# Kernel optimization log

Hardware: AMD Instinct MI355X
Metric: run time of the kernel (lower is better)

The kernel has to match this reference:

```python
import jax, jax.numpy as jnp
import numpy as np
from math import factorial

# ---- static config mirroring Cace.__init__ ----
MAX_L = 3            # max angular degree
N_RBF = 8            # Bessel radial basis size
RB = 8               # n_radial_basis (radial embedding dim after transform)
K = 3                # n_atom_basis -> edge channels C = K*K
NZ = 4               # len(zs)
CUTOFF = 5.5
N_NODES = 2000
N_EDGES = 50000
T_MP = 1             # num_message_passing
MP_NORM = 1.0 / np.sqrt(25.0)   # 1/sqrt(avg_num_neighbors)
C = K * K

def _lxlylz(max_l):
    out = []
    for l in range(max_l + 1):
        for lx in range(l, -1, -1):
            for ly in range(l - lx, -1, -1):
                out.append((lx, ly, l - lx - ly))
    return out

L_LIST = _lxlylz(MAX_L)                 # 20 Cartesian monomials for max_l=3
NL = len(L_LIST)
LX = np.array([t[0] for t in L_LIST]); LY = np.array([t[1] for t in L_LIST]); LZ = np.array([t[2] for t in L_LIST])
DEGS = LX + LY + LZ                     # degree l of each monomial
MULTI = np.array([factorial(int(d)) / (factorial(int(a)) * factorial(int(b)) * factorial(int(c)))
                  for a, b, c, d in zip(LX, LY, LZ, DEGS)], dtype=np.float32)
SEL = np.zeros((NL, MAX_L + 1), np.float32)
SEL[np.arange(NL), DEGS] = 1.0          # monomial -> degree one-hot (for per-l sums)
NB = 1 + (MAX_L + 1)                    # symmetrizer feats: nu=1 (l=0) + nu=2 per l

def bessel(r):  # [E] -> [E, N_RBF]
    n = jnp.arange(1, N_RBF + 1, dtype=r.dtype)
    return jnp.sqrt(2.0 / CUTOFF) * jnp.sin(n[None, :] * jnp.pi * r[:, None] / CUTOFF) / r[:, None]

def poly_cutoff(r):  # MACE-style polynomial cutoff, p=6
    p = 6.0
    u = r / CUTOFF
    f = 1.0 - (p + 1.0) * (p + 2.0) / 2.0 * u**6 + p * (p + 2.0) * u**7 - p * (p + 1.0) / 2.0 * u**8
    return f * (u < 1.0)

def axis_pows(x):  # [E] -> [E, MAX_L+1] = x^0..x^MAX_L (safe grads, handles negatives)
    pows = [jnp.ones_like(x)]
    for _ in range(MAX_L):
        pows.append(pows[-1] * x)
    return jnp.stack(pows, axis=1)

def angular(u):  # unit vectors [E,3] -> Cartesian monomials [E, NL]
    return axis_pows(u[:, 0])[:, LX] * axis_pows(u[:, 1])[:, LY] * axis_pows(u[:, 2])[:, LZ]

def radial_transform(x, W):  # x [N,R,L,C], W [MAX_L+1,R,Rb] shared per degree l
    return jnp.einsum('nrlc,lrb->nblc', x, W[DEGS])

def symmetrize(A):  # A [N,Rb,NL,C] -> B [N,Rb,NB,C]
    b1 = A[:, :, :1, :]  # nu=1: the (0,0,0) monomial (index 0)
    w = (A * A) * jnp.asarray(MULTI)[None, None, :, None]
    b2 = jnp.einsum('nrlc,lm->nrmc', w, jnp.asarray(SEL))  # nu=2 invariant per degree l
    return jnp.concatenate([b1, b2], axis=2)


def setup_inputs() -> dict:
    key = jax.random.key(0)
    ks = jax.random.split(key, 9)
    positions = jax.random.uniform(ks[0], (N_NODES, 3), dtype=jnp.float32) * 12.0
    species = jax.random.randint(ks[1], (N_NODES,), 0, NZ)
    send = jax.random.randint(ks[2], (N_EDGES,), 0, N_NODES)
    off = jax.random.randint(ks[3], (N_EDGES,), 1, N_NODES)
    recv = (send + off) % N_NODES  # no self-edges -> strictly positive edge lengths
    edge_index = jnp.stack([send, recv])
    shifts = jnp.zeros((N_EDGES, 3), jnp.float32)
    W_embed = jax.random.normal(ks[4], (NZ, K), jnp.float32)
    W_radial = jax.random.normal(ks[5], (MAX_L + 1, N_RBF, RB), jnp.float32) / np.sqrt(N_RBF)
    W_mem = jax.random.normal(ks[6], (MAX_L + 1, RB, RB), jnp.float32) / np.sqrt(RB)
    W_ar = jax.random.normal(ks[7], (N_RBF, RB), jnp.float32) / np.sqrt(N_RBF)
    W_chi = jax.random.normal(ks[8], (RB, NB), jnp.float32) * 0.1
    return {"positions": positions, "shifts": shifts, "W_embed": W_embed, "W_radial": W_radial,
            "W_mem": W_mem, "W_ar": W_ar, "W_chi": W_chi, "species": species, "edge_index": edge_index}


def reference(positions, shifts, W_embed, W_radial, W_mem, W_ar, W_chi, species, edge_index):
    n_nodes = positions.shape[0]
    send, recv = edge_index[0], edge_index[1]
    # edge geometry
    vec = positions[recv] - positions[send] + shifts
    lengths = jnp.linalg.norm(vec, axis=-1)
    u = vec / (lengths[:, None] + 1e-9)
    rad = bessel(lengths)          # [E,R]
    fcut = poly_cutoff(lengths)    # [E]
    ang = angular(u)               # [E,NL]
    # edge type encoding: outer product of sender/receiver species embeddings
    emb = W_embed[species]         # [N,K]
    enc = (emb[send][:, :, None] * emb[recv][:, None, :]).reshape(-1, C)  # [E,C]
    # elementwise_multiply_3tensors -> [E,R,NL,C]
    edge_attri = jnp.einsum('er,el,ec->erlc', rad * fcut[:, None], ang, enc)
    A = radial_transform(jax.ops.segment_sum(edge_attri, recv, num_segments=n_nodes), W_radial)  # [N,Rb,NL,C]
    B = symmetrize(A)              # [N,Rb,NB,C]
    feats = [B]
    for _ in range(T_MP):
        mem = jnp.einsum('nrlc,lrb->nblc', A, W_mem[DEGS])        # NodeMemory
        chi = jnp.einsum('nbkc,bk->nc', B, W_chi)                  # MessageBchi node scalar
        msg_bchi = edge_attri * chi[send][:, None, None, :]
        A_bchi = radial_transform(jax.ops.segment_sum(msg_bchi, recv, num_segments=n_nodes), W_radial)
        fr = (rad @ W_ar) * fcut[:, None]                          # MessageAr radial filter [E,Rb]
        msg_ar = A[send] * fr[:, :, None, None]
        A_ar = jax.ops.segment_sum(msg_ar, recv, num_segments=n_nodes)
        A = (A_ar + A_bchi) * MP_NORM + mem
        B = symmetrize(A)
        feats.append(B)
    return jnp.stack(feats, axis=-1)   # [N,Rb,NB,C,T_MP+1]
```

## Files before the change

kernel.cpp:

```cpp
#include <hip/hip_runtime.h>
#include <hip/hip_bf16.h>


#define CUTF 5.5f
#define MPNORM 0.2f

__constant__ int   d_DEGS[20]  = {0,1,1,1,2,2,2,2,2,2,3,3,3,3,3,3,3,3,3,3};
__constant__ float d_MULTI[20] = {1,1,1,1,1,2,2,1,2,1,1,3,3,3,6,3,1,3,3,1};

__global__ __launch_bounds__(1024) void k_prep(const int* __restrict__ eidx,
                                               int* __restrict__ offs,
                                               int* __restrict__ cursor,
                                               int N, int E) {
  __shared__ int cnt[2048];
  __shared__ int part[1024];
  int t = threadIdx.x;
  cnt[t] = 0; cnt[t + 1024] = 0;
  for (int i = t; i < N; i += 1024) cursor[i] = 0;
  __syncthreads();
  const int* recv = eidx + E;
  if ((E & 3) == 0) {
    #pragma unroll 2
    for (int i = t * 4; i + 3 < E; i += 4096) {
      int4 v = *reinterpret_cast<const int4*>(recv + i);
      atomicAdd(&cnt[v.x], 1); atomicAdd(&cnt[v.y], 1);
      atomicAdd(&cnt[v.z], 1); atomicAdd(&cnt[v.w], 1);
    }
  } else {
    #pragma unroll 4
    for (int i = t; i < E; i += 1024) atomicAdd(&cnt[recv[i]], 1);
  }
  __syncthreads();
  int a = cnt[2 * t], b = cnt[2 * t + 1];
  int s = a + b;
  part[t] = s;
  __syncthreads();
  for (int d = 1; d < 1024; d <<= 1) {
    int add = (t >= d) ? part[t - d] : 0;
    __syncthreads();
    part[t] += add;
    __syncthreads();
  }
  int excl = part[t] - s;
  if (2 * t     < N) offs[2 * t]     = excl;
  if (2 * t + 1 < N) offs[2 * t + 1] = excl + a;
  if (t == 1023) offs[N] = part[1023];
}

__global__ void k_edge(const float* __restrict__ pos,
                       const float* __restrict__ shifts,
                       const float* __restrict__ Wemb,
                       const float* __restrict__ War,
                       const int* __restrict__ species,
                       const int* __restrict__ eidx,
                       const int* __restrict__ offs,
                       int* __restrict__ cursor,
                       float* __restrict__ edata,
                       int* __restrict__ esend,
                       int E) {
  __shared__ float war_s[64];
  int t = threadIdx.x;
  if (t < 64) war_s[t] = War[t];
  __syncthreads();
  int e = blockIdx.x * blockDim.x + t;
  if (e >= E) return;
  int s  = eidx[e];
  int rI = eidx[E + e];
  float vx = pos[rI*3+0] - pos[s*3+0] + shifts[e*3+0];
  float vy = pos[rI*3+1] - pos[s*3+1] + shifts[e*3+1];
  float vz = pos[rI*3+2] - pos[s*3+2] + shifts[e*3+2];
  float len = sqrtf(vx*vx + vy*vy + vz*vz);
  float inv = 1.0f / (len + 1e-9f);
  float ux = vx*inv, uy = vy*inv, uz = vz*inv;
  float uu = len * (1.0f/CUTF);
  float u2 = uu*uu, u6 = u2*u2*u2;
  float fcut = (uu < 1.0f) ? (1.0f - 28.0f*u6 + 48.0f*u6*uu - 21.0f*u6*u2) : 0.0f;
  float x = 3.14159265358979f * uu;
  float sn = sinf(x), c2 = 2.0f*cosf(x), snm1 = 0.0f;
  float pref = sqrtf(2.0f/CUTF) / (len + 1e-20f);
  float rad[8];
  float v[48];
  #pragma unroll
  for (int k = 0; k < 8; k++) {
    rad[k] = pref * sn;
    v[k]   = rad[k] * fcut;
    float nxt = c2*sn - snm1; snm1 = sn; sn = nxt;
  }
  #pragma unroll
  for (int b = 0; b < 8; b++) {
    float a = 0.0f;
    #pragma unroll
    for (int k = 0; k < 8; k++) a += rad[k] * war_s[k*8+b];
    v[8+b] = a * fcut;
  }
  float px2 = ux*ux, py2 = uy*uy, pz2 = uz*uz;
  v[16] = 1.0f; v[17] = ux;     v[18] = uy;     v[19] = uz;
  v[20] = px2;  v[21] = ux*uy;  v[22] = ux*uz;  v[23] = py2;
  v[24] = uy*uz;v[25] = pz2;
  v[26] = px2*ux; v[27] = px2*uy; v[28] = px2*uz; v[29] = ux*py2;
  v[30] = ux*uy*uz; v[31] = ux*pz2; v[32] = py2*uy; v[33] = py2*uz;
  v[34] = uy*pz2; v[35] = pz2*uz;
  int zs = species[s], zr = species[rI];
  float es0 = Wemb[zs*3+0], es1 = Wemb[zs*3+1], es2 = Wemb[zs*3+2];
  float er0 = Wemb[zr*3+0], er1 = Wemb[zr*3+1], er2 = Wemb[zr*3+2];
  v[36] = es0*er0; v[37] = es0*er1; v[38] = es0*er2;
  v[39] = es1*er0; v[40] = es1*er1; v[41] = es1*er2;
  v[42] = es2*er0; v[43] = es2*er1; v[44] = es2*er2;
  v[45] = 0.0f; v[46] = 0.0f; v[47] = 0.0f;
  int slot = atomicAdd(&cursor[rI], 1);
  int dst = offs[rI] + slot;
  float4* eb4 = reinterpret_cast<float4*>(edata + (size_t)dst * 48);
  #pragma unroll
  for (int w = 0; w < 12; w++)
    eb4[w] = make_float4(v[4*w], v[4*w+1], v[4*w+2], v[4*w+3]);
  esend[dst] = s;
}

__global__ __launch_bounds__(192) void k_nodeA(
    const float* __restrict__ edata, const int* __restrict__ offs,
    const float* __restrict__ Wrad, const float* __restrict__ Wchi,
    float* __restrict__ A, uint4* __restrict__ Abf2,
    float* __restrict__ chi, float* __restrict__ B0, int N) {
  __shared__ float wr_s[288];
  __shared__ float wchi_s[40];
  __shared__ float Bsh[360];
  int t = threadIdx.x, n = blockIdx.x;
  for (int i = t; i < 256; i += 192) { int d = i >> 6, rm = i & 63; wr_s[d*72+rm] = Wrad[i]; }
  for (int i = t; i < 40;  i += 192) wchi_s[i] = Wchi[i];
  for (int i = t; i < 360; i += 192) Bsh[i] = 0.0f;
  int l = t / 9, c = t - l*9;
  bool act = t < 180;
  int ll = act ? l : 0, cc = act ? c : 0;
  float acc[8];
  #pragma unroll
  for (int r = 0; r < 8; r++) acc[r] = 0.0f;
  int start = offs[n], end = offs[n+1];
  #pragma unroll 4
  for (int j = start; j < end; j++) {
    const float* row = edata + (size_t)j * 48;
    float p = row[16+ll] * row[36+cc];
    #pragma unroll
    for (int r = 0; r < 8; r++) acc[r] += row[r] * p;
  }
  __syncthreads();
  int deg = act ? d_DEGS[ll] : 0;
  const float* wp = &wr_s[deg*72];
  float Ab[8];
  #pragma unroll
  for (int b = 0; b < 8; b++) {
    float a = 0.0f;
    #pragma unroll
    for (int r = 0; r < 8; r++) a += acc[r] * wp[r*8+b];
    Ab[b] = a;
  }
  if (act) {
    #pragma unroll
    for (int b = 0; b < 8; b++) A[(size_t)n*1440 + t*8 + b] = Ab[b];
    unsigned int pk[4];
    #pragma unroll
    for (int bp = 0; bp < 4; bp++) {
      __hip_bfloat16 blo = __float2bfloat16(Ab[2*bp]);
      __hip_bfloat16 bhi = __float2bfloat16(Ab[2*bp+1]);
      pk[bp] = (unsigned int)(*reinterpret_cast<unsigned short*>(&blo))
             | ((unsigned int)(*reinterpret_cast<unsigned short*>(&bhi)) << 16);
    }
    uint4 q; q.x = pk[0]; q.y = pk[1]; q.z = pk[2]; q.w = pk[3];
    Abf2[(size_t)n*180 + t] = q;
    if (l == 0) {
      #pragma unroll
      for (int b = 0; b < 8; b++) Bsh[b*45 + c] = Ab[b];
    }
    float mlt = d_MULTI[ll]; int kk = 1 + deg;
    #pragma unroll
    for (int b = 0; b < 8; b++) atomicAdd(&Bsh[b*45 + kk*9 + c], mlt*Ab[b]*Ab[b]);
  }
  __syncthreads();
  if (t < 9) {
    float s = 0.0f;
    for (int b = 0; b < 8; b++)
      #pragma unroll
      for (int kq = 0; kq < 5; kq++) s += Bsh[b*45 + kq*9 + t] * wchi_s[b*5 + kq];
    chi[n*9 + t] = s;
  }
  for (int i = t; i < 360; i += 192)
    B0[(size_t)n*360 + i] = Bsh[i];
}

__global__ __launch_bounds__(192) void k_node2(
    const float* __restrict__ edata, const int* __restrict__ esend,
    const int* __restrict__ offs,
    const float* __restrict__ Wrad, const float* __restrict__ Wmem,
    const float* __restrict__ A, const uint4* __restrict__ Abf2,
    const float* __restrict__ chi, const float* __restrict__ B0,
    float* __restrict__ out, int N) {
  __shared__ float wr_s[288], wm_s[288];
  __shared__ float Bsh[360];
  int t = threadIdx.x, n = blockIdx.x;
  for (int i = t; i < 256; i += 192) {
    int d = i >> 6, rm = i & 63;
    wr_s[d*72+rm] = Wrad[i];
    wm_s[d*72+rm] = Wmem[i];
  }
  for (int i = t; i < 360; i += 192) Bsh[i] = 0.0f;
  int l = t / 9, c = t - l*9;
  bool act = t < 180;
  int ll = act ? l : 0, cc = act ? c : 0;
  int tt = act ? t : 0;
  float Sacc[8], ARacc[8];
  #pragma unroll
  for (int r = 0; r < 8; r++) { Sacc[r] = 0.0f; ARacc[r] = 0.0f; }
  int start = offs[n], end = offs[n+1];
  #pragma unroll 4
  for (int j = start; j < end; j++) {
    const float* row = edata + (size_t)j * 48;
    int snd = esend[j];
    float ch = chi[snd*9 + cc];
    float pch = row[16+ll] * row[36+cc] * ch;
    #pragma unroll
    for (int r = 0; r < 8; r++) Sacc[r] += row[r] * pch;
    const uint4 q = Abf2[(size_t)snd*180 + tt];
    float a0 = __uint_as_float(q.x << 16), a1 = __uint_as_float(q.x & 0xffff0000u);
    float a2 = __uint_as_float(q.y << 16), a3 = __uint_as_float(q.y & 0xffff0000u);
    float a4 = __uint_as_float(q.z << 16), a5 = __uint_as_float(q.z & 0xffff0000u);
    float a6 = __uint_as_float(q.w << 16), a7 = __uint_as_float(q.w & 0xffff0000u);
    ARacc[0] += a0*row[8];  ARacc[1] += a1*row[9];
    ARacc[2] += a2*row[10]; ARacc[3] += a3*row[11];
    ARacc[4] += a4*row[12]; ARacc[5] += a5*row[13];
    ARacc[6] += a6*row[14]; ARacc[7] += a7*row[15];
  }
  __syncthreads();
  if (act) {
    int deg = d_DEGS[ll];
    const float* wrp = &wr_s[deg*72];
    const float* wmp = &wm_s[deg*72];
    const float* aop = A + (size_t)n*1440 + t*8;
    float aown[8];
    #pragma unroll
    for (int r = 0; r < 8; r++) aown[r] = aop[r];
    float newA[8];
    #pragma unroll
    for (int b = 0; b < 8; b++) {
      float mem = 0.0f, ab = 0.0f;
      #pragma unroll
      for (int r = 0; r < 8; r++) { mem += aown[r]*wmp[r*8+b]; ab += Sacc[r]*wrp[r*8+b]; }
      newA[b] = (ARacc[b] + ab)*MPNORM + mem;
    }
    if (l == 0) {
      #pragma unroll
      for (int b = 0; b < 8; b++) Bsh[b*45 + c] = newA[b];
    }
    float mlt = d_MULTI[ll]; int kk = 1 + deg;
    #pragma unroll
    for (int b = 0; b < 8; b++) atomicAdd(&Bsh[b*45 + kk*9 + c], mlt*newA[b]*newA[b]);
  }
  __syncthreads();
  float2* out2 = reinterpret_cast<float2*>(out);
  for (int i = t; i < 360; i += 192) {
    float2 pk; pk.x = B0[(size_t)n*360 + i]; pk.y = Bsh[i];
    out2[(size_t)n*360 + i] = pk;
  }
}

extern "C" void kernel_launch(void* const* d_in, const int* in_sizes, int n_in,
                              void* d_out, int out_size, void* d_ws, size_t ws_size,
                              hipStream_t stream) {
  const float* pos    = (const float*)d_in[0];
  const float* shifts = (const float*)d_in[1];
  const float* Wemb   = (const float*)d_in[2];
  const float* Wrad   = (const float*)d_in[3];
  const float* Wmem   = (const float*)d_in[4];
  const float* War    = (const float*)d_in[5];
  const float* Wchi   = (const float*)d_in[6];
  const int* species = (const int*)d_in[7];
  const int* eidx    = (const int*)d_in[8];
  float* out = (float*)d_out;
  int N = in_sizes[7];
  int E = in_sizes[8] / 2;

  char* base = (char*)d_ws;
  size_t off = 0;
  float* edata = (float*)(base + off); off += (size_t)E*48*4;
  float* A     = (float*)(base + off); off += (size_t)N*1440*4;
  uint4* Abf2  = (uint4*)(base + off); off += (size_t)N*180*16;
  float* chi   = (float*)(base + off); off += (size_t)N*9*4;
  float* B0    = (float*)(base + off); off += (size_t)N*360*4;
  int* cursor  = (int*)(base + off);   off += (size_t)N*4;
  int* offs    = (int*)(base + off);   off += (((size_t)(N+1)*4) + 15) & ~(size_t)15;
  int* esend   = (int*)(base + off);   off += (size_t)E*4;

  int eb = (E + 255) / 256;
  k_prep<<<1, 1024, 0, stream>>>(eidx, offs, cursor, N, E);
  k_edge<<<eb, 256, 0, stream>>>(pos, shifts, Wemb, War, species, eidx, offs, cursor,
                                 edata, esend, E);
  k_nodeA<<<N, 192, 0, stream>>>(edata, offs, Wrad, Wchi, A, Abf2, chi, B0, N);
  k_node2<<<N, 192, 0, stream>>>(edata, esend, offs, Wrad, Wmem, A, Abf2, chi, B0, out, N);
}
```

Baseline: 151.8 us.

## Fuse node passes into one cooperative kernel with grid sync and register-held A

Replaces the two node kernels with a single cooperative kernel. Each block handles two nodes, keeps their A values in registers across a grid-wide sync, and writes both B outputs as packed float2 at the end. This removes one launch, the fp32 A round trip and the B0 round trip through global memory. In exchange it depends on every block being co-resident (1000 blocks of 192 threads), adds grid-barrier cost, and keeps the two-kernel path as a fallback.

```diff
diff --git a/kernel.cpp b/kernel.cpp
--- a/kernel.cpp
+++ b/kernel.cpp
@@ -1,9 +1,12 @@
 #include <hip/hip_runtime.h>
 #include <hip/hip_bf16.h>
+#include <hip/hip_cooperative_groups.h>
 
 
 #define CUTF 5.5f
 #define MPNORM 0.2f
+
+namespace cg = cooperative_groups;
 
 __constant__ int   d_DEGS[20]  = {0,1,1,1,2,2,2,2,2,2,3,3,3,3,3,3,3,3,3,3};
 __constant__ float d_MULTI[20] = {1,1,1,1,1,2,2,1,2,1,1,3,3,3,6,3,1,3,3,1};
@@ -116,6 +119,149 @@
   esend[dst] = s;
 }
 
+__global__ __launch_bounds__(192, 3) void k_nodeF(
+    const float* __restrict__ edata, const int* __restrict__ esend,
+    const int* __restrict__ offs,
+    const float* __restrict__ Wrad, const float* __restrict__ Wmem,
+    const float* __restrict__ Wchi,
+    uint4* __restrict__ Abf2, float* __restrict__ chi,
+    float* __restrict__ out, int N, int G) {
+  __shared__ float wr_s[288], wm_s[288];
+  __shared__ float wchi_s[40];
+  __shared__ float Bsh1[2][360];
+  __shared__ float Bsh2[360];
+  int t = threadIdx.x;
+  for (int i = t; i < 256; i += 192) {
+    int d = i >> 6, rm = i & 63;
+    wr_s[d*72+rm] = Wrad[i];
+    wm_s[d*72+rm] = Wmem[i];
+  }
+  for (int i = t; i < 40;  i += 192) wchi_s[i] = Wchi[i];
+  for (int i = t; i < 720; i += 192) (&Bsh1[0][0])[i] = 0.0f;
+  int l = t / 9, c = t - l*9;
+  bool act = t < 180;
+  int ll = act ? l : 0, cc = act ? c : 0;
+  int tt = act ? t : 0;
+  int deg = d_DEGS[ll];
+  float mlt = d_MULTI[ll];
+  int kk1 = 1 + deg;
+  __syncthreads();
+
+  float AbK[2][8];
+  #pragma unroll
+  for (int q = 0; q < 2; q++) {
+    int n = blockIdx.x + q * G;
+    if (n < N) {
+      float acc[8];
+      #pragma unroll
+      for (int r = 0; r < 8; r++) acc[r] = 0.0f;
+      int start = offs[n], end = offs[n+1];
+      #pragma unroll 4
+      for (int j = start; j < end; j++) {
+        const float* row = edata + (size_t)j * 48;
+        float p = row[16+ll] * row[36+cc];
+        #pragma unroll
+        for (int r = 0; r < 8; r++) acc[r] += row[r] * p;
+      }
+      const float* wp = &wr_s[deg*72];
+      #pragma unroll
+      for (int b = 0; b < 8; b++) {
+        float a = 0.0f;
+        #pragma unroll
+        for (int r = 0; r < 8; r++) a += acc[r] * wp[r*8+b];
+        AbK[q][b] = a;
+      }
+      if (act) {
+        unsigned int pk[4];
+        #pragma unroll
+        for (int bp = 0; bp < 4; bp++) {
+          __hip_bfloat16 blo = __float2bfloat16(AbK[q][2*bp]);
+          __hip_bfloat16 bhi = __float2bfloat16(AbK[q][2*bp+1]);
+          pk[bp] = (unsigned int)(*reinterpret_cast<unsigned short*>(&blo))
+                 | ((unsigned int)(*reinterpret_cast<unsigned short*>(&bhi)) << 16);
+        }
+        uint4 qq; qq.x = pk[0]; qq.y = pk[1]; qq.z = pk[2]; qq.w = pk[3];
+        Abf2[(size_t)n*180 + t] = qq;
+        if (l == 0) {
+          #pragma unroll
+          for (int b = 0; b < 8; b++) Bsh1[q][b*45 + c] = AbK[q][b];
+        }
+        #pragma unroll
+        for (int b = 0; b < 8; b++)
+          atomicAdd(&Bsh1[q][b*45 + kk1*9 + c], mlt*AbK[q][b]*AbK[q][b]);
+      }
+    }
+    __syncthreads();
+    if (n < N && t < 9) {
+      float s = 0.0f;
+      for (int b = 0; b < 8; b++)
+        #pragma unroll
+        for (int kq = 0; kq < 5; kq++) s += Bsh1[q][b*45 + kq*9 + t] * wchi_s[b*5 + kq];
+      chi[n*9 + t] = s;
+    }
+  }
+  __threadfence();
+  cg::this_grid().sync();
+  #pragma unroll
+  for (int q = 0; q < 2; q++) {
+    int n = blockIdx.x + q * G;
+    for (int i = t; i < 360; i += 192) Bsh2[i] = 0.0f;
+    __syncthreads();
+    if (n < N) {
+      float Sacc[8], ARacc[8];
+      #pragma unroll
+      for (int r = 0; r < 8; r++) { Sacc[r] = 0.0f; ARacc[r] = 0.0f; }
+      int start = offs[n], end = offs[n+1];
+      #pragma unroll 4
+      for (int j = start; j < end; j++) {
+        const float* row = edata + (size_t)j * 48;
+        int snd = esend[j];
+        float ch = chi[snd*9 + cc];
+        float pch = row[16+ll] * row[36+cc] * ch;
+        #pragma unroll
+        for (int r = 0; r < 8; r++) Sacc[r] += row[r] * pch;
+        const uint4 qv = Abf2[(size_t)snd*180 + tt];
+        float a0 = __uint_as_float(qv.x << 16), a1 = __uint_as_float(qv.x & 0xffff0000u);
+        float a2 = __uint_as_float(qv.y << 16), a3 = __uint_as_float(qv.y & 0xffff0000u);
+        float a4 = __uint_as_float(qv.z << 16), a5 = __uint_as_float(qv.z & 0xffff0000u);
+        float a6 = __uint_as_float(qv.w << 16), a7 = __uint_as_float(qv.w & 0xffff0000u);
+        ARacc[0] += a0*row[8];  ARacc[1] += a1*row[9];
+        ARacc[2] += a2*row[10]; ARacc[3] += a3*row[11];
+        ARacc[4] += a4*row[12]; ARacc[5] += a5*row[13];
+        ARacc[6] += a6*row[14]; ARacc[7] += a7*row[15];
+      }
+      if (act) {
+        const float* wrp = &wr_s[deg*72];
+        const float* wmp = &wm_s[deg*72];
+        float newA[8];
+        #pragma unroll
+        for (int b = 0; b < 8; b++) {
+          float mem = 0.0f, ab = 0.0f;
+          #pragma unroll
+          for (int r = 0; r < 8; r++) { mem += AbK[q][r]*wmp[r*8+b]; ab += Sacc[r]*wrp[r*8+b]; }
+          newA[b] = (ARacc[b] + ab)*MPNORM + mem;
+        }
+        if (l == 0) {
+          #pragma unroll
+          for (int b = 0; b < 8; b++) Bsh2[b*45 + c] = newA[b];
+        }
+        #pragma unroll
+        for (int b = 0; b < 8; b++)
+          atomicAdd(&Bsh2[b*45 + kk1*9 + c], mlt*newA[b]*newA[b]);
+      }
+    }
+    __syncthreads();
+    if (n < N) {
+      float2* out2 = reinterpret_cast<float2*>(out);
+      for (int i = t; i < 360; i += 192) {
+        float2 pk2; pk2.x = Bsh1[q][i]; pk2.y = Bsh2[i];
+        out2[(size_t)n*360 + i] = pk2;
+      }
+    }
+    __syncthreads();
+  }
+}
+
 __global__ __launch_bounds__(192) void k_nodeA(
     const float* __restrict__ edata, const int* __restrict__ offs,
     const float* __restrict__ Wrad, const float* __restrict__ Wchi,
@@ -164,8 +310,8 @@
       pk[bp] = (unsigned int)(*reinterpret_cast<unsigned short*>(&blo))
              | ((unsigned int)(*reinterpret_cast<unsigned short*>(&bhi)) << 16);
     }
-    uint4 q; q.x = pk[0]; q.y = pk[1]; q.z = pk[2]; q.w = pk[3];
-    Abf2[(size_t)n*180 + t] = q;
+    uint4 qv; qv.x = pk[0]; qv.y = pk[1]; qv.z = pk[2]; qv.w = pk[3];
+    Abf2[(size_t)n*180 + t] = qv;
     if (l == 0) {
       #pragma unroll
       for (int b = 0; b < 8; b++) Bsh[b*45 + c] = Ab[b];
@@ -218,11 +364,11 @@
     float pch = row[16+ll] * row[36+cc] * ch;
     #pragma unroll
     for (int r = 0; r < 8; r++) Sacc[r] += row[r] * pch;
-    const uint4 q = Abf2[(size_t)snd*180 + tt];
-    float a0 = __uint_as_float(q.x << 16), a1 = __uint_as_float(q.x & 0xffff0000u);
-    float a2 = __uint_as_float(q.y << 16), a3 = __uint_as_float(q.y & 0xffff0000u);
-    float a4 = __uint_as_float(q.z << 16), a5 = __uint_as_float(q.z & 0xffff0000u);
-    float a6 = __uint_as_float(q.w << 16), a7 = __uint_as_float(q.w & 0xffff0000u);
+    const uint4 qv = Abf2[(size_t)snd*180 + tt];
+    float a0 = __uint_as_float(qv.x << 16), a1 = __uint_as_float(qv.x & 0xffff0000u);
+    float a2 = __uint_as_float(qv.y << 16), a3 = __uint_as_float(qv.y & 0xffff0000u);
+    float a4 = __uint_as_float(qv.z << 16), a5 = __uint_as_float(qv.z & 0xffff0000u);
+    float a6 = __uint_as_float(qv.w << 16), a7 = __uint_as_float(qv.w & 0xffff0000u);
     ARacc[0] += a0*row[8];  ARacc[1] += a1*row[9];
     ARacc[2] += a2*row[10]; ARacc[3] += a3*row[11];
     ARacc[4] += a4*row[12]; ARacc[5] += a5*row[13];
@@ -288,10 +434,39 @@
   int* offs    = (int*)(base + off);   off += (((size_t)(N+1)*4) + 15) & ~(size_t)15;
   int* esend   = (int*)(base + off);   off += (size_t)E*4;
 
+  int G = (N + 1) / 2;
+
+  static int s_coop = -1;
+  static int s_G = 0;
+  if (s_coop < 0) {
+    int dev = 0; hipGetDevice(&dev);
+    int nCU = 0;
+    hipDeviceGetAttribute(&nCU, hipDeviceAttributeMultiprocessorCount, dev);
+    int maxB = 0;
+    hipError_t oe = hipOccupancyMaxActiveBlocksPerMultiprocessor(
+        &maxB, reinterpret_cast<const void*>(k_nodeF), 192, 0);
+    s_coop = (oe == hipSuccess && nCU > 0 && (long)maxB * nCU >= G) ? 1 : 0;
+    s_G = G;
+  }
+  if (s_G != G) s_coop = 0;
+
   int eb = (E + 255) / 256;
   k_prep<<<1, 1024, 0, stream>>>(eidx, offs, cursor, N, E);
   k_edge<<<eb, 256, 0, stream>>>(pos, shifts, Wemb, War, species, eidx, offs, cursor,
                                  edata, esend, E);
-  k_nodeA<<<N, 192, 0, stream>>>(edata, offs, Wrad, Wchi, A, Abf2, chi, B0, N);
-  k_node2<<<N, 192, 0, stream>>>(edata, esend, offs, Wrad, Wmem, A, Abf2, chi, B0, out, N);
-}
+
+  bool done = false;
+  if (s_coop == 1) {
+    void* args[] = {(void*)&edata, (void*)&esend, (void*)&offs,
+                    (void*)&Wrad, (void*)&Wmem, (void*)&Wchi,
+                    (void*)&Abf2, (void*)&chi, (void*)&out,
+                    (void*)&N, (void*)&G};
+    hipError_t le = hipLaunchCooperativeKernel(
+        reinterpret_cast<void*>(k_nodeF), dim3(G), dim3(192), args, 0, stream);
+    if (le == hipSuccess) done = true; else s_coop = 0;
+  }
+  if (!done) {
+    k_nodeA<<<N, 192, 0, stream>>>(edata, offs, Wrad, Wchi, A, Abf2, chi, B0, N);
+    k_node2<<<N, 192, 0, stream>>>(edata, esend, offs, Wrad, Wmem, A, Abf2, chi, B0, out, N);
+  }
+}
```

Measured after the change: 152.0 us. Within noise of the previous version (+0.1%).

## Precompute edge ranks in prep, shrink edge blocks, process two nodes per block

Applied to the files above, without the earlier changes.

The histogram pass now stores each edge's rank within its receiver bucket, so the edge kernel computes its CSR slot directly instead of doing a global atomic on a cursor array. That also removes the cursor zeroing. The edge kernel moves to 64-thread blocks. Both node kernels now handle two nodes per block with interleaved gather loops, which halves block count and gives each thread two independent load streams to hide latency. The cost is more register pressure, an extra erank array write and read, and per-block imbalance when the two nodes have different degrees.

```diff
diff --git a/kernel.cpp b/kernel.cpp
--- a/kernel.cpp
+++ b/kernel.cpp
@@ -10,25 +10,25 @@
 
 __global__ __launch_bounds__(1024) void k_prep(const int* __restrict__ eidx,
                                                int* __restrict__ offs,
-                                               int* __restrict__ cursor,
+                                               int* __restrict__ erank,
                                                int N, int E) {
   __shared__ int cnt[2048];
   __shared__ int part[1024];
   int t = threadIdx.x;
   cnt[t] = 0; cnt[t + 1024] = 0;
-  for (int i = t; i < N; i += 1024) cursor[i] = 0;
   __syncthreads();
   const int* recv = eidx + E;
   if ((E & 3) == 0) {
-    #pragma unroll 2
     for (int i = t * 4; i + 3 < E; i += 4096) {
       int4 v = *reinterpret_cast<const int4*>(recv + i);
-      atomicAdd(&cnt[v.x], 1); atomicAdd(&cnt[v.y], 1);
-      atomicAdd(&cnt[v.z], 1); atomicAdd(&cnt[v.w], 1);
+      int r0 = atomicAdd(&cnt[v.x], 1);
+      int r1 = atomicAdd(&cnt[v.y], 1);
+      int r2 = atomicAdd(&cnt[v.z], 1);
+      int r3 = atomicAdd(&cnt[v.w], 1);
+      *reinterpret_cast<int4*>(erank + i) = make_int4(r0, r1, r2, r3);
     }
   } else {
-    #pragma unroll 4
-    for (int i = t; i < E; i += 1024) atomicAdd(&cnt[recv[i]], 1);
+    for (int i = t; i < E; i += 1024) erank[i] = atomicAdd(&cnt[recv[i]], 1);
   }
   __syncthreads();
   int a = cnt[2 * t], b = cnt[2 * t + 1];
@@ -47,25 +47,27 @@
   if (t == 1023) offs[N] = part[1023];
 }
 
-__global__ void k_edge(const float* __restrict__ pos,
+__global__ __launch_bounds__(64) void k_edge(
+                       const float* __restrict__ pos,
                        const float* __restrict__ shifts,
                        const float* __restrict__ Wemb,
                        const float* __restrict__ War,
                        const int* __restrict__ species,
                        const int* __restrict__ eidx,
                        const int* __restrict__ offs,
-                       int* __restrict__ cursor,
+                       const int* __restrict__ erank,
                        float* __restrict__ edata,
                        int* __restrict__ esend,
                        int E) {
   __shared__ float war_s[64];
   int t = threadIdx.x;
-  if (t < 64) war_s[t] = War[t];
-  __syncthreads();
-  int e = blockIdx.x * blockDim.x + t;
+  war_s[t] = War[t];
+  __syncthreads();
+  int e = blockIdx.x * 64 + t;
   if (e >= E) return;
   int s  = eidx[e];
   int rI = eidx[E + e];
+  int rk = erank[e];
   float vx = pos[rI*3+0] - pos[s*3+0] + shifts[e*3+0];
   float vy = pos[rI*3+1] - pos[s*3+1] + shifts[e*3+1];
   float vz = pos[rI*3+2] - pos[s*3+2] + shifts[e*3+2];
@@ -107,8 +109,7 @@
   v[39] = es1*er0; v[40] = es1*er1; v[41] = es1*er2;
   v[42] = es2*er0; v[43] = es2*er1; v[44] = es2*er2;
   v[45] = 0.0f; v[46] = 0.0f; v[47] = 0.0f;
-  int slot = atomicAdd(&cursor[rI], 1);
-  int dst = offs[rI] + slot;
+  int dst = offs[rI] + rk;
   float4* eb4 = reinterpret_cast<float4*>(edata + (size_t)dst * 48);
   #pragma unroll
   for (int w = 0; w < 12; w++)
@@ -123,67 +124,98 @@
     float* __restrict__ chi, float* __restrict__ B0, int N) {
   __shared__ float wr_s[288];
   __shared__ float wchi_s[40];
-  __shared__ float Bsh[360];
-  int t = threadIdx.x, n = blockIdx.x;
+  __shared__ float Bsh[2][360];
+  int t = threadIdx.x;
+  int n0 = blockIdx.x * 2, n1 = n0 + 1;
   for (int i = t; i < 256; i += 192) { int d = i >> 6, rm = i & 63; wr_s[d*72+rm] = Wrad[i]; }
   for (int i = t; i < 40;  i += 192) wchi_s[i] = Wchi[i];
-  for (int i = t; i < 360; i += 192) Bsh[i] = 0.0f;
+  for (int i = t; i < 720; i += 192) (&Bsh[0][0])[i] = 0.0f;
   int l = t / 9, c = t - l*9;
   bool act = t < 180;
   int ll = act ? l : 0, cc = act ? c : 0;
-  float acc[8];
-  #pragma unroll
-  for (int r = 0; r < 8; r++) acc[r] = 0.0f;
-  int start = offs[n], end = offs[n+1];
+  int s0 = offs[n0], m0 = offs[n0+1];
+  int m1 = (n1 < N) ? offs[n0+2] : m0;
+  int L0 = m0 - s0, L1 = m1 - m0;
+  int Lc = (L0 < L1) ? L0 : L1;
+  float acc0[8], acc1[8];
+  #pragma unroll
+  for (int r = 0; r < 8; r++) { acc0[r] = 0.0f; acc1[r] = 0.0f; }
+  #pragma unroll 2
+  for (int i = 0; i < Lc; i++) {
+    const float* r0 = edata + (size_t)(s0+i) * 48;
+    const float* r1 = edata + (size_t)(m0+i) * 48;
+    float p0 = r0[16+ll] * r0[36+cc];
+    float p1 = r1[16+ll] * r1[36+cc];
+    #pragma unroll
+    for (int r = 0; r < 8; r++) { acc0[r] += r0[r] * p0; acc1[r] += r1[r] * p1; }
+  }
   #pragma unroll 4
-  for (int j = start; j < end; j++) {
-    const float* row = edata + (size_t)j * 48;
-    float p = row[16+ll] * row[36+cc];
-    #pragma unroll
-    for (int r = 0; r < 8; r++) acc[r] += row[r] * p;
+  for (int i = Lc; i < L0; i++) {
+    const float* r0 = edata + (size_t)(s0+i) * 48;
+    float p0 = r0[16+ll] * r0[36+cc];
+    #pragma unroll
+    for (int r = 0; r < 8; r++) acc0[r] += r0[r] * p0;
+  }
+  #pragma unroll 4
+  for (int i = Lc; i < L1; i++) {
+    const float* r1 = edata + (size_t)(m0+i) * 48;
+    float p1 = r1[16+ll] * r1[36+cc];
+    #pragma unroll
+    for (int r = 0; r < 8; r++) acc1[r] += r1[r] * p1;
   }
   __syncthreads();
   int deg = act ? d_DEGS[ll] : 0;
+  float mlt = d_MULTI[ll]; int kk = 1 + deg;
   const float* wp = &wr_s[deg*72];
-  float Ab[8];
-  #pragma unroll
-  for (int b = 0; b < 8; b++) {
-    float a = 0.0f;
-    #pragma unroll
-    for (int r = 0; r < 8; r++) a += acc[r] * wp[r*8+b];
-    Ab[b] = a;
-  }
-  if (act) {
-    #pragma unroll
-    for (int b = 0; b < 8; b++) A[(size_t)n*1440 + t*8 + b] = Ab[b];
-    unsigned int pk[4];
-    #pragma unroll
-    for (int bp = 0; bp < 4; bp++) {
-      __hip_bfloat16 blo = __float2bfloat16(Ab[2*bp]);
-      __hip_bfloat16 bhi = __float2bfloat16(Ab[2*bp+1]);
-      pk[bp] = (unsigned int)(*reinterpret_cast<unsigned short*>(&blo))
-             | ((unsigned int)(*reinterpret_cast<unsigned short*>(&bhi)) << 16);
-    }
-    uint4 q; q.x = pk[0]; q.y = pk[1]; q.z = pk[2]; q.w = pk[3];
-    Abf2[(size_t)n*180 + t] = q;
-    if (l == 0) {
-      #pragma unroll
-      for (int b = 0; b < 8; b++) Bsh[b*45 + c] = Ab[b];
-    }
-    float mlt = d_MULTI[ll]; int kk = 1 + deg;
-    #pragma unroll
-    for (int b = 0; b < 8; b++) atomicAdd(&Bsh[b*45 + kk*9 + c], mlt*Ab[b]*Ab[b]);
-  }
-  __syncthreads();
-  if (t < 9) {
-    float s = 0.0f;
-    for (int b = 0; b < 8; b++)
-      #pragma unroll
-      for (int kq = 0; kq < 5; kq++) s += Bsh[b*45 + kq*9 + t] * wchi_s[b*5 + kq];
-    chi[n*9 + t] = s;
-  }
-  for (int i = t; i < 360; i += 192)
-    B0[(size_t)n*360 + i] = Bsh[i];
+  #pragma unroll
+  for (int q = 0; q < 2; q++) {
+    int n = n0 + q;
+    if (n >= N) break;
+    const float* ac = q ? acc1 : acc0;
+    float Ab[8];
+    #pragma unroll
+    for (int b = 0; b < 8; b++) {
+      float a = 0.0f;
+      #pragma unroll
+      for (int r = 0; r < 8; r++) a += ac[r] * wp[r*8+b];
+      Ab[b] = a;
+    }
+    if (act) {
+      #pragma unroll
+      for (int b = 0; b < 8; b++) A[(size_t)n*1440 + t*8 + b] = Ab[b];
+      unsigned int pk[4];
+      #pragma unroll
+      for (int bp = 0; bp < 4; bp++) {
+        __hip_bfloat16 blo = __float2bfloat16(Ab[2*bp]);
+        __hip_bfloat16 bhi = __float2bfloat16(Ab[2*bp+1]);
+        pk[bp] = (unsigned int)(*reinterpret_cast<unsigned short*>(&blo))
+               | ((unsigned int)(*reinterpret_cast<unsigned short*>(&bhi)) << 16);
+      }
+      uint4 qv; qv.x = pk[0]; qv.y = pk[1]; qv.z = pk[2]; qv.w = pk[3];
+      Abf2[(size_t)n*180 + t] = qv;
+      if (l == 0) {
+        #pragma unroll
+        for (int b = 0; b < 8; b++) Bsh[q][b*45 + c] = Ab[b];
+      }
+      #pragma unroll
+      for (int b = 0; b < 8; b++) atomicAdd(&Bsh[q][b*45 + kk*9 + c], mlt*Ab[b]*Ab[b]);
+    }
+  }
+  __syncthreads();
+  if (t < 18) {
+    int q = t / 9, tc = t - q*9;
+    int n = n0 + q;
+    if (n < N) {
+      float s = 0.0f;
+      for (int b = 0; b < 8; b++)
+        #pragma unroll
+        for (int kq = 0; kq < 5; kq++) s += Bsh[q][b*45 + kq*9 + tc] * wchi_s[b*5 + kq];
+      chi[n*9 + tc] = s;
+    }
+  }
+  int tot = (n1 < N) ? 720 : 360;
+  for (int i = t; i < tot; i += 192)
+    B0[(size_t)n0*360 + i] = (&Bsh[0][0])[i];
 }
 
 __global__ __launch_bounds__(192) void k_node2(
@@ -194,70 +226,126 @@
     const float* __restrict__ chi, const float* __restrict__ B0,
     float* __restrict__ out, int N) {
   __shared__ float wr_s[288], wm_s[288];
-  __shared__ float Bsh[360];
-  int t = threadIdx.x, n = blockIdx.x;
+  __shared__ float Bsh[2][360];
+  int t = threadIdx.x;
+  int n0 = blockIdx.x * 2, n1 = n0 + 1;
   for (int i = t; i < 256; i += 192) {
     int d = i >> 6, rm = i & 63;
     wr_s[d*72+rm] = Wrad[i];
     wm_s[d*72+rm] = Wmem[i];
   }
-  for (int i = t; i < 360; i += 192) Bsh[i] = 0.0f;
+  for (int i = t; i < 720; i += 192) (&Bsh[0][0])[i] = 0.0f;
   int l = t / 9, c = t - l*9;
   bool act = t < 180;
   int ll = act ? l : 0, cc = act ? c : 0;
   int tt = act ? t : 0;
-  float Sacc[8], ARacc[8];
-  #pragma unroll
-  for (int r = 0; r < 8; r++) { Sacc[r] = 0.0f; ARacc[r] = 0.0f; }
-  int start = offs[n], end = offs[n+1];
+  int s0 = offs[n0], m0 = offs[n0+1];
+  int m1 = (n1 < N) ? offs[n0+2] : m0;
+  int L0 = m0 - s0, L1 = m1 - m0;
+  int Lc = (L0 < L1) ? L0 : L1;
+  float S0[8], R0[8], S1[8], R1[8];
+  #pragma unroll
+  for (int r = 0; r < 8; r++) { S0[r]=0.0f; R0[r]=0.0f; S1[r]=0.0f; R1[r]=0.0f; }
+  #pragma unroll 2
+  for (int i = 0; i < Lc; i++) {
+    int j0 = s0 + i, j1 = m0 + i;
+    const float* r0 = edata + (size_t)j0 * 48;
+    const float* r1 = edata + (size_t)j1 * 48;
+    int sd0 = esend[j0], sd1 = esend[j1];
+    float ch0 = chi[sd0*9 + cc], ch1 = chi[sd1*9 + cc];
+    const uint4 q0 = Abf2[(size_t)sd0*180 + tt];
+    const uint4 q1 = Abf2[(size_t)sd1*180 + tt];
+    float pc0 = r0[16+ll] * r0[36+cc] * ch0;
+    float pc1 = r1[16+ll] * r1[36+cc] * ch1;
+    #pragma unroll
+    for (int r = 0; r < 8; r++) { S0[r] += r0[r] * pc0; S1[r] += r1[r] * pc1; }
+    float a0 = __uint_as_float(q0.x << 16), a1 = __uint_as_float(q0.x & 0xffff0000u);
+    float a2 = __uint_as_float(q0.y << 16), a3 = __uint_as_float(q0.y & 0xffff0000u);
+    float a4 = __uint_as_float(q0.z << 16), a5 = __uint_as_float(q0.z & 0xffff0000u);
+    float a6 = __uint_as_float(q0.w << 16), a7 = __uint_as_float(q0.w & 0xffff0000u);
+    R0[0] += a0*r0[8];  R0[1] += a1*r0[9];  R0[2] += a2*r0[10]; R0[3] += a3*r0[11];
+    R0[4] += a4*r0[12]; R0[5] += a5*r0[13]; R0[6] += a6*r0[14]; R0[7] += a7*r0[15];
+    float b0 = __uint_as_float(q1.x << 16), b1 = __uint_as_float(q1.x & 0xffff0000u);
+    float b2 = __uint_as_float(q1.y << 16), b3 = __uint_as_float(q1.y & 0xffff0000u);
+    float b4 = __uint_as_float(q1.z << 16), b5 = __uint_as_float(q1.z & 0xffff0000u);
+    float b6 = __uint_as_float(q1.w << 16), b7 = __uint_as_float(q1.w & 0xffff0000u);
+    R1[0] += b0*r1[8];  R1[1] += b1*r1[9];  R1[2] += b2*r1[10]; R1[3] += b3*r1[11];
+    R1[4] += b4*r1[12]; R1[5] += b5*r1[13]; R1[6] += b6*r1[14]; R1[7] += b7*r1[15];
+  }
   #pragma unroll 4
-  for (int j = start; j < end; j++) {
-    const float* row = edata + (size_t)j * 48;
-    int snd = esend[j];
-    float ch = chi[snd*9 + cc];
-    float pch = row[16+ll] * row[36+cc] * ch;
-    #pragma unroll
-    for (int r = 0; r < 8; r++) Sacc[r] += row[r] * pch;
-    const uint4 q = Abf2[(size_t)snd*180 + tt];
-    float a0 = __uint_as_float(q.x << 16), a1 = __uint_as_float(q.x & 0xffff0000u);
-    float a2 = __uint_as_float(q.y << 16), a3 = __uint_as_float(q.y & 0xffff0000u);
-    float a4 = __uint_as_float(q.z << 16), a5 = __uint_as_float(q.z & 0xffff0000u);
-    float a6 = __uint_as_float(q.w << 16), a7 = __uint_as_float(q.w & 0xffff0000u);
-    ARacc[0] += a0*row[8];  ARacc[1] += a1*row[9];
-    ARacc[2] += a2*row[10]; ARacc[3] += a3*row[11];
-    ARacc[4] += a4*row[12]; ARacc[5] += a5*row[13];
-    ARacc[6] += a6*row[14]; ARacc[7] += a7*row[15];
-  }
-  __syncthreads();
-  if (act) {
-    int deg = d_DEGS[ll];
-    const float* wrp = &wr_s[deg*72];
-    const float* wmp = &wm_s[deg*72];
-    const float* aop = A + (size_t)n*1440 + t*8;
-    float aown[8];
-    #pragma unroll
-    for (int r = 0; r < 8; r++) aown[r] = aop[r];
-    float newA[8];
-    #pragma unroll
-    for (int b = 0; b < 8; b++) {
-      float mem = 0.0f, ab = 0.0f;
-      #pragma unroll
-      for (int r = 0; r < 8; r++) { mem += aown[r]*wmp[r*8+b]; ab += Sacc[r]*wrp[r*8+b]; }
-      newA[b] = (ARacc[b] + ab)*MPNORM + mem;
-    }
-    if (l == 0) {
-      #pragma unroll
-      for (int b = 0; b < 8; b++) Bsh[b*45 + c] = newA[b];
-    }
-    float mlt = d_MULTI[ll]; int kk = 1 + deg;
-    #pragma unroll
-    for (int b = 0; b < 8; b++) atomicAdd(&Bsh[b*45 + kk*9 + c], mlt*newA[b]*newA[b]);
+  for (int i = Lc; i < L0; i++) {
+    int j0 = s0 + i;
+    const float* r0 = edata + (size_t)j0 * 48;
+    int sd0 = esend[j0];
+    float ch0 = chi[sd0*9 + cc];
+    const uint4 q0 = Abf2[(size_t)sd0*180 + tt];
+    float pc0 = r0[16+ll] * r0[36+cc] * ch0;
+    #pragma unroll
+    for (int r = 0; r < 8; r++) S0[r] += r0[r] * pc0;
+    float a0 = __uint_as_float(q0.x << 16), a1 = __uint_as_float(q0.x & 0xffff0000u);
+    float a2 = __uint_as_float(q0.y << 16), a3 = __uint_as_float(q0.y & 0xffff0000u);
+    float a4 = __uint_as_float(q0.z << 16), a5 = __uint_as_float(q0.z & 0xffff0000u);
+    float a6 = __uint_as_float(q0.w << 16), a7 = __uint_as_float(q0.w & 0xffff0000u);
+    R0[0] += a0*r0[8];  R0[1] += a1*r0[9];  R0[2] += a2*r0[10]; R0[3] += a3*r0[11];
+    R0[4] += a4*r0[12]; R0[5] += a5*r0[13]; R0[6] += a6*r0[14]; R0[7] += a7*r0[15];
+  }
+  #pragma unroll 4
+  for (int i = Lc; i < L1; i++) {
+    int j1 = m0 + i;
+    const float* r1 = edata + (size_t)j1 * 48;
+    int sd1 = esend[j1];
+    float ch1 = chi[sd1*9 + cc];
+    const uint4 q1 = Abf2[(size_t)sd1*180 + tt];
+    float pc1 = r1[16+ll] * r1[36+cc] * ch1;
+    #pragma unroll
+    for (int r = 0; r < 8; r++) S1[r] += r1[r] * pc1;
+    float b0 = __uint_as_float(q1.x << 16), b1 = __uint_as_float(q1.x & 0xffff0000u);
+    float b2 = __uint_as_float(q1.y << 16), b3 = __uint_as_float(q1.y & 0xffff0000u);
+    float b4 = __uint_as_float(q1.z << 16), b5 = __uint_as_float(q1.z & 0xffff0000u);
+    float b6 = __uint_as_float(q1.w << 16), b7 = __uint_as_float(q1.w & 0xffff0000u);
+    R1[0] += b0*r1[8];  R1[1] += b1*r1[9];  R1[2] += b2*r1[10]; R1[3] += b3*r1[11];
+    R1[4] += b4*r1[12]; R1[5] += b5*r1[13]; R1[6] += b6*r1[14]; R1[7] += b7*r1[15];
+  }
+  __syncthreads();
+  int deg = act ? d_DEGS[ll] : 0;
+  float mlt = d_MULTI[ll]; int kk = 1 + deg;
+  const float* wrp = &wr_s[deg*72];
+  const float* wmp = &wm_s[deg*72];
+  #pragma unroll
+  for (int q = 0; q < 2; q++) {
+    int n = n0 + q;
+    if (n >= N) break;
+    if (act) {
+      const float* Sq = q ? S1 : S0;
+      const float* Rq = q ? R1 : R0;
+      const float* aop = A + (size_t)n*1440 + t*8;
+      float aown[8];
+      #pragma unroll
+      for (int r = 0; r < 8; r++) aown[r] = aop[r];
+      float newA[8];
+      #pragma unroll
+      for (int b = 0; b < 8; b++) {
+        float mem = 0.0f, ab = 0.0f;
+        #pragma unroll
+        for (int r = 0; r < 8; r++) { mem += aown[r]*wmp[r*8+b]; ab += Sq[r]*wrp[r*8+b]; }
+        newA[b] = (Rq[b] + ab)*MPNORM + mem;
+      }
+      if (l == 0) {
+        #pragma unroll
+        for (int b = 0; b < 8; b++) Bsh[q][b*45 + c] = newA[b];
+      }
+      #pragma unroll
+      for (int b = 0; b < 8; b++) atomicAdd(&Bsh[q][b*45 + kk*9 + c], mlt*newA[b]*newA[b]);
+    }
   }
   __syncthreads();
   float2* out2 = reinterpret_cast<float2*>(out);
-  for (int i = t; i < 360; i += 192) {
-    float2 pk; pk.x = B0[(size_t)n*360 + i]; pk.y = Bsh[i];
-    out2[(size_t)n*360 + i] = pk;
+  int tot = (n1 < N) ? 720 : 360;
+  for (int i = t; i < tot; i += 192) {
+    float2 pk;
+    pk.x = B0[(size_t)n0*360 + i];
+    pk.y = (&Bsh[0][0])[i];
+    out2[(size_t)n0*360 + i] = pk;
   }
 }
 
@@ -284,14 +372,14 @@
   uint4* Abf2  = (uint4*)(base + off); off += (size_t)N*180*16;
   float* chi   = (float*)(base + off); off += (size_t)N*9*4;
   float* B0    = (float*)(base + off); off += (size_t)N*360*4;
-  int* cursor  = (int*)(base + off);   off += (size_t)N*4;
   int* offs    = (int*)(base + off);   off += (((size_t)(N+1)*4) + 15) & ~(size_t)15;
   int* esend   = (int*)(base + off);   off += (size_t)E*4;
-
-  int eb = (E + 255) / 256;
-  k_prep<<<1, 1024, 0, stream>>>(eidx, offs, cursor, N, E);
-  k_edge<<<eb, 256, 0, stream>>>(pos, shifts, Wemb, War, species, eidx, offs, cursor,
-                                 edata, esend, E);
-  k_nodeA<<<N, 192, 0, stream>>>(edata, offs, Wrad, Wchi, A, Abf2, chi, B0, N);
-  k_node2<<<N, 192, 0, stream>>>(edata, esend, offs, Wrad, Wmem, A, Abf2, chi, B0, out, N);
-}
+  int* erank   = (int*)(base + off);   off += (((size_t)E*4) + 15) & ~(size_t)15;
+
+  int G = (N + 1) / 2;
+  k_prep<<<1, 1024, 0, stream>>>(eidx, offs, erank, N, E);
+  k_edge<<<(E + 63) / 64, 64, 0, stream>>>(pos, shifts, Wemb, War, species, eidx,
+                                           offs, erank, edata, esend, E);
+  k_nodeA<<<G, 192, 0, stream>>>(edata, offs, Wrad, Wchi, A, Abf2, chi, B0, N);
+  k_node2<<<G, 192, 0, stream>>>(edata, esend, offs, Wrad, Wmem, A, Abf2, chi, B0, out, N);
+}
```

Measured after the change: 150.7 us. No clear change (-0.7%).
